# Kernel tuning notes

Measured on AMD Instinct MI355X. Metric: run time of the kernel, lower is better.

Reference implementation:

```python
import jax, jax.numpy as jnp
import numpy as np

N_NODES = 50000
N_EDGES = 800000
NFEAT = 96
NHID = 128
EPS = 1e-12  # F.normalize default eps


def setup_inputs() -> dict:
    key = jax.random.key(0)
    k1, k2, k3, k4 = jax.random.split(key, 4)
    edge_index = jax.random.randint(k1, (2, N_EDGES), 0, N_NODES, dtype=jnp.int64)
    x = jax.random.normal(k2, (N_NODES, NFEAT), dtype=jnp.float32)
    # Glorot-ish scaling for linear weights
    W_l = jax.random.normal(k3, (NHID, NFEAT), dtype=jnp.float32) * (1.0 / np.sqrt(NFEAT))
    b_l = jnp.zeros((NHID,), dtype=jnp.float32)
    W_r = jax.random.normal(k4, (NHID, NFEAT), dtype=jnp.float32) * (1.0 / np.sqrt(NFEAT))
    return {"edge_index": edge_index, "x": x, "W_l": W_l, "b_l": b_l, "W_r": W_r}


def reference(edge_index, x, W_l, b_l, W_r):
    # PyG SAGEConv, aggr='mean', root_weight=True, normalize=True
    src, dst = edge_index[0], edge_index[1]
    # gather source features, scatter-sum into destination nodes
    msg_sum = jax.ops.segment_sum(x[src], dst, num_segments=N_NODES)  # [N, nfeat]
    deg = jax.ops.segment_sum(jnp.ones((edge_index.shape[1],), dtype=x.dtype),
                              dst, num_segments=N_NODES)
    agg = msg_sum / jnp.maximum(deg, 1.0)[:, None]  # mean; isolated nodes -> 0
    out = agg @ W_l.T + b_l + x @ W_r.T  # [N, nhid]
    # L2 normalize per node (F.normalize p=2, dim=-1)
    norm = jnp.linalg.norm(out, axis=-1, keepdims=True)
    return out / jnp.maximum(norm, EPS)
```

## Files before the change

### kernel.cpp

```cpp
#include <hip/hip_runtime.h>


typedef __attribute__((ext_vector_type(8))) short short8;
typedef __attribute__((ext_vector_type(4))) float floatx4;

constexpr int kNodes = 50000;
constexpr int kEdges = 800000;
constexpr int kF = 96;
constexpr int kH = 128;
constexpr int kEllW = 32;
constexpr int kSpillCap = 4096;
constexpr int kBktRange = kNodes / 8;

constexpr size_t kXhOff    = 0;
constexpr size_t kAggOff   = 9600000;
constexpr size_t kWhOff    = 19200000;
constexpr size_t kEllOff   = 19249152;
constexpr size_t kCurOff   = 22449152;
constexpr size_t kSpcOff   = 22649152;
constexpr size_t kSpillOff = 22649168;

constexpr int kPeriods    = 782;
constexpr int kMegaBlocks = kPeriods * 11;
constexpr int kPrepBlocks = kPeriods * 3;
constexpr int kPrepItems  = kNodes * kF / 8 + kH * 192 / 8;
constexpr int kPrepStride = kPrepBlocks * 256;

__device__ __forceinline__ unsigned pack2_bf16(float a, float b) {
  unsigned ua = __float_as_uint(a), ub = __float_as_uint(b);
  ua = (ua + 0x7fffu + ((ua >> 16) & 1u)) >> 16;
  ub = (ub + 0x7fffu + ((ub >> 16) & 1u)) >> 16;
  return ua | (ub << 16);
}
__device__ __forceinline__ float bf_lo(unsigned u) { return __uint_as_float(u << 16); }
__device__ __forceinline__ float bf_hi(unsigned u) { return __uint_as_float(u & 0xffff0000u); }

__device__ __forceinline__ void ell_insert(int dst, int src, int* cursor,
                                           ushort* ell, unsigned* spill,
                                           int* spillCnt) {
  const int slot = atomicAdd(&cursor[dst], 1);
  if (slot < kEllW) {
    ell[(size_t)dst * kEllW + slot] = (ushort)src;
  } else {
    const int sp = atomicAdd(spillCnt, 1);
    if (sp < kSpillCap) spill[sp] = ((unsigned)dst << 16) | (unsigned)src;
  }
}

__global__ void __launch_bounds__(256)
mega_kernel(const int* __restrict__ ei, const float* __restrict__ x,
            const float* __restrict__ Wl, const float* __restrict__ Wr,
            uint4* __restrict__ xh4, uint4* __restrict__ wh4,
            int* __restrict__ cursor, ushort* __restrict__ ell,
            unsigned* __restrict__ spill, int* __restrict__ spillCnt) {
  const int p = blockIdx.x / 11;
  const int r = blockIdx.x % 11;
  if (r < 8) {
    const int g = r;
    const int lo = g * kBktRange, hi = lo + kBktRange;
    const int base = p * 1024 + threadIdx.x;
    int d[4];
#pragma unroll
    for (int k = 0; k < 4; ++k) {
      const int e = base + k * 256;
      d[k] = (e < kEdges) ? ei[kEdges + e] : -1;
    }
#pragma unroll
    for (int k = 0; k < 4; ++k) {
      if (d[k] >= lo && d[k] < hi) {
        const int e = base + k * 256;
        ell_insert(d[k], ei[e], cursor, ell, spill, spillCnt);
      }
    }
    return;
  }
  constexpr int kCvt = kNodes * kF / 8;
  const int pid = p * 3 + (r - 8);
  for (int i = pid * 256 + threadIdx.x; i < kPrepItems; i += kPrepStride) {
    if (i < kCvt) {
      const float4 v0 = reinterpret_cast<const float4*>(x)[i * 2];
      const float4 v1 = reinterpret_cast<const float4*>(x)[i * 2 + 1];
      uint4 o;
      o.x = pack2_bf16(v0.x, v0.y);
      o.y = pack2_bf16(v0.z, v0.w);
      o.z = pack2_bf16(v1.x, v1.y);
      o.w = pack2_bf16(v1.z, v1.w);
      xh4[i] = o;
    } else {
      const int j = i - kCvt;
      const int row = j / 24, chunk = j % 24;
      const float* src = (chunk < 12) ? (Wl + (size_t)row * kF + chunk * 8)
                                      : (Wr + (size_t)row * kF + (chunk - 12) * 8);
      const float4 v0 = reinterpret_cast<const float4*>(src)[0];
      const float4 v1 = reinterpret_cast<const float4*>(src)[1];
      uint4 o;
      o.x = pack2_bf16(v0.x, v0.y);
      o.y = pack2_bf16(v0.z, v0.w);
      o.z = pack2_bf16(v1.x, v1.y);
      o.w = pack2_bf16(v1.z, v1.w);
      wh4[j] = o;
    }
  }
}

__global__ void __launch_bounds__(256)
gather_kernel(const uint4* __restrict__ xh4, const int* __restrict__ cursor,
              const ushort* __restrict__ ell, const unsigned* __restrict__ spill,
              const int* __restrict__ spillCnt, uint4* __restrict__ aggh4) {
  const int wave = threadIdx.x >> 6, lane = threadIdx.x & 63;
  const int slot = lane / 12;
  const int c = lane % 12;
  const bool gactive = lane < 48;
  const int sc = min(*spillCnt, kSpillCap);
  const int g = blockIdx.x & 7;
  const int j = blockIdx.x >> 3;
  const int stride = (gridDim.x >> 3) * 8;
  const int hi = (g + 1) * kBktRange;

  for (int nA = g * kBktRange + j * 8 + wave * 2; nA < hi; nA += stride) {
    const int nB = nA + 1;
    const bool hasB = nB < hi;
    const int degA = cursor[nA];
    const int degB = hasB ? cursor[nB] : 0;
    const int dmA = min(degA, kEllW);
    const int dmB = min(degB, kEllW);
    const ushort* __restrict__ erowA = ell + (size_t)nA * kEllW;
    const ushort* __restrict__ erowB = ell + (size_t)nB * kEllW;

    float a0 = 0.f, a1 = 0.f, a2 = 0.f, a3 = 0.f,
          a4 = 0.f, a5 = 0.f, a6 = 0.f, a7 = 0.f;
    float b0 = 0.f, b1 = 0.f, b2 = 0.f, b3 = 0.f,
          b4 = 0.f, b5 = 0.f, b6 = 0.f, b7 = 0.f;

    int sA[8], sB[8];
#pragma unroll
    for (int t = 0; t < 8; ++t) {
      const int idx = (t << 2) + slot;
      sA[t] = (gactive && idx < dmA) ? (int)erowA[idx] : -1;
      sB[t] = (gactive && idx < dmB) ? (int)erowB[idx] : -1;
    }
#pragma unroll
    for (int t = 0; t < 8; ++t) {
      if (sA[t] >= 0) {
        const uint4 v = xh4[(size_t)sA[t] * 12 + c];
        a0 += bf_lo(v.x); a1 += bf_hi(v.x);
        a2 += bf_lo(v.y); a3 += bf_hi(v.y);
        a4 += bf_lo(v.z); a5 += bf_hi(v.z);
        a6 += bf_lo(v.w); a7 += bf_hi(v.w);
      }
      if (sB[t] >= 0) {
        const uint4 v = xh4[(size_t)sB[t] * 12 + c];
        b0 += bf_lo(v.x); b1 += bf_hi(v.x);
        b2 += bf_lo(v.y); b3 += bf_hi(v.y);
        b4 += bf_lo(v.z); b5 += bf_hi(v.z);
        b6 += bf_lo(v.w); b7 += bf_hi(v.w);
      }
    }
    for (int jj = 0; jj < sc; ++jj) {
      const unsigned pr = spill[jj];
      const int pd = (int)(pr >> 16);
      if (lane < 12 && (pd == nA || (hasB && pd == nB))) {
        const uint4 v = xh4[(size_t)(pr & 0xffffu) * 12 + c];
        if (pd == nA) {
          a0 += bf_lo(v.x); a1 += bf_hi(v.x);
          a2 += bf_lo(v.y); a3 += bf_hi(v.y);
          a4 += bf_lo(v.z); a5 += bf_hi(v.z);
          a6 += bf_lo(v.w); a7 += bf_hi(v.w);
        } else {
          b0 += bf_lo(v.x); b1 += bf_hi(v.x);
          b2 += bf_lo(v.y); b3 += bf_hi(v.y);
          b4 += bf_lo(v.z); b5 += bf_hi(v.z);
          b6 += bf_lo(v.w); b7 += bf_hi(v.w);
        }
      }
    }
    a0 += __shfl(a0, lane + 24, 64); a1 += __shfl(a1, lane + 24, 64);
    a2 += __shfl(a2, lane + 24, 64); a3 += __shfl(a3, lane + 24, 64);
    a4 += __shfl(a4, lane + 24, 64); a5 += __shfl(a5, lane + 24, 64);
    a6 += __shfl(a6, lane + 24, 64); a7 += __shfl(a7, lane + 24, 64);
    a0 += __shfl(a0, lane + 12, 64); a1 += __shfl(a1, lane + 12, 64);
    a2 += __shfl(a2, lane + 12, 64); a3 += __shfl(a3, lane + 12, 64);
    a4 += __shfl(a4, lane + 12, 64); a5 += __shfl(a5, lane + 12, 64);
    a6 += __shfl(a6, lane + 12, 64); a7 += __shfl(a7, lane + 12, 64);
    b0 += __shfl(b0, lane + 24, 64); b1 += __shfl(b1, lane + 24, 64);
    b2 += __shfl(b2, lane + 24, 64); b3 += __shfl(b3, lane + 24, 64);
    b4 += __shfl(b4, lane + 24, 64); b5 += __shfl(b5, lane + 24, 64);
    b6 += __shfl(b6, lane + 24, 64); b7 += __shfl(b7, lane + 24, 64);
    b0 += __shfl(b0, lane + 12, 64); b1 += __shfl(b1, lane + 12, 64);
    b2 += __shfl(b2, lane + 12, 64); b3 += __shfl(b3, lane + 12, 64);
    b4 += __shfl(b4, lane + 12, 64); b5 += __shfl(b5, lane + 12, 64);
    b6 += __shfl(b6, lane + 12, 64); b7 += __shfl(b7, lane + 12, 64);

    if (lane < 12) {
      const float invA = 1.0f / fmaxf((float)degA, 1.0f);
      uint4 o;
      o.x = pack2_bf16(a0 * invA, a1 * invA);
      o.y = pack2_bf16(a2 * invA, a3 * invA);
      o.z = pack2_bf16(a4 * invA, a5 * invA);
      o.w = pack2_bf16(a6 * invA, a7 * invA);
      aggh4[(size_t)nA * 12 + c] = o;
      if (hasB) {
        const float invB = 1.0f / fmaxf((float)degB, 1.0f);
        uint4 p;
        p.x = pack2_bf16(b0 * invB, b1 * invB);
        p.y = pack2_bf16(b2 * invB, b3 * invB);
        p.z = pack2_bf16(b4 * invB, b5 * invB);
        p.w = pack2_bf16(b6 * invB, b7 * invB);
        aggh4[(size_t)nB * 12 + c] = p;
      }
    }
  }
}

__global__ void __launch_bounds__(256)
mfma_kernel(const uint4* __restrict__ xh4, const uint4* __restrict__ aggh4,
            const uint4* __restrict__ wh4, const float* __restrict__ bl,
            float* __restrict__ out) {
  const int wave = threadIdx.x >> 6, lane = threadIdx.x & 63;
  const int tile = blockIdx.x * 4 + wave;
  if (tile >= kNodes / 16) return;
  const int base = tile * 16;
  const int r = lane & 15, q = lane >> 4;

  const short8* aggS = reinterpret_cast<const short8*>(aggh4);
  const short8* xhS  = reinterpret_cast<const short8*>(xh4);
  const short8* whS  = reinterpret_cast<const short8*>(wh4);

  floatx4 acc[8] = {};
#pragma unroll
  for (int ks = 0; ks < 6; ++ks) {
    const short8* Ab = (ks < 3) ? aggS : xhS;
    const int chunk = (ks < 3 ? ks * 4 : (ks - 3) * 4) + q;
    const short8 a = Ab[(size_t)(base + r) * 12 + chunk];
#pragma unroll
    for (int cg = 0; cg < 8; ++cg) {
      const short8 b = whS[(cg * 16 + r) * 24 + ks * 4 + q];
      acc[cg] = __builtin_amdgcn_mfma_f32_16x16x32_bf16(a, b, acc[cg], 0, 0, 0);
    }
  }

  float p0 = 0.f, p1 = 0.f, p2 = 0.f, p3 = 0.f;
#pragma unroll
  for (int cg = 0; cg < 8; ++cg) {
    const float bb = bl[cg * 16 + r];
    acc[cg][0] += bb; acc[cg][1] += bb; acc[cg][2] += bb; acc[cg][3] += bb;
    p0 += acc[cg][0] * acc[cg][0];
    p1 += acc[cg][1] * acc[cg][1];
    p2 += acc[cg][2] * acc[cg][2];
    p3 += acc[cg][3] * acc[cg][3];
  }
#pragma unroll
  for (int off = 1; off < 16; off <<= 1) {
    p0 += __shfl_xor(p0, off, 64);
    p1 += __shfl_xor(p1, off, 64);
    p2 += __shfl_xor(p2, off, 64);
    p3 += __shfl_xor(p3, off, 64);
  }
  const float s0 = 1.0f / fmaxf(sqrtf(p0), 1e-12f);
  const float s1 = 1.0f / fmaxf(sqrtf(p1), 1e-12f);
  const float s2 = 1.0f / fmaxf(sqrtf(p2), 1e-12f);
  const float s3 = 1.0f / fmaxf(sqrtf(p3), 1e-12f);

#pragma unroll
  for (int cg = 0; cg < 8; ++cg) {
    const int col = cg * 16 + r;
    float* o = out + (size_t)(base + q * 4) * kH + col;
    o[0 * kH] = acc[cg][0] * s0;
    o[1 * kH] = acc[cg][1] * s1;
    o[2 * kH] = acc[cg][2] * s2;
    o[3 * kH] = acc[cg][3] * s3;
  }
}

extern "C" void kernel_launch(void* const* d_in, const int* in_sizes, int n_in,
                              void* d_out, int out_size, void* d_ws, size_t ws_size,
                              hipStream_t stream) {
  const int*   ei = (const int*)d_in[0];
  const float* x  = (const float*)d_in[1];
  const float* Wl = (const float*)d_in[2];
  const float* bl = (const float*)d_in[3];
  const float* Wr = (const float*)d_in[4];
  float* out = (float*)d_out;

  char* ws = (char*)d_ws;
  uint4*    xh4      = (uint4*)(ws + kXhOff);
  uint4*    aggh4    = (uint4*)(ws + kAggOff);
  uint4*    wh4      = (uint4*)(ws + kWhOff);
  ushort*   ell      = (ushort*)(ws + kEllOff);
  int*      cursor   = (int*)(ws + kCurOff);
  int*      spillCnt = (int*)(ws + kSpcOff);
  unsigned* spill    = (unsigned*)(ws + kSpillOff);

  hipMemsetAsync(ws + kCurOff, 0, 200008, stream);

  mega_kernel<<<kMegaBlocks, 256, 0, stream>>>(ei, x, Wl, Wr, xh4, wh4, cursor,
                                               ell, spill, spillCnt);

  gather_kernel<<<391 * 8, 256, 0, stream>>>(xh4, cursor, ell, spill, spillCnt,
                                             aggh4);

  constexpr int tiles = kNodes / 16;
  mfma_kernel<<<(tiles + 3) / 4, 256, 0, stream>>>(xh4, aggh4, wh4, bl, out);
}
```

Measured before the change: 112.6 us.

## Fuse neighbor gather into MFMA kernel via per-wave LDS aggregate tile

Merges the gather and MFMA kernels: each wave aggregates neighbor means for its 16-node tile into a padded shared-memory buffer, then feeds those rows straight into the bf16 MFMA projection. This removes one kernel launch and the round trip of the aggregated bf16 tensor through global memory. In exchange, the gather loses its node-bucketed scheduling, which may have aimed at cache locality, the grid shrinks to one block per 64 nodes, and LDS use per block could reduce occupancy.

```diff
diff --git a/kernel.cpp b/kernel.cpp
--- a/kernel.cpp
+++ b/kernel.cpp
@@ -13,7 +13,6 @@
 constexpr int kBktRange = kNodes / 8;
 
 constexpr size_t kXhOff    = 0;
-constexpr size_t kAggOff   = 9600000;
 constexpr size_t kWhOff    = 19200000;
 constexpr size_t kEllOff   = 19249152;
 constexpr size_t kCurOff   = 22449152;
@@ -25,6 +24,8 @@
 constexpr int kPrepBlocks = kPeriods * 3;
 constexpr int kPrepItems  = kNodes * kF / 8 + kH * 192 / 8;
 constexpr int kPrepStride = kPrepBlocks * 256;
+
+constexpr int kRowS = 104;
 
 __device__ __forceinline__ unsigned pack2_bf16(float a, float b) {
   unsigned ua = __float_as_uint(a), ub = __float_as_uint(b);
@@ -104,24 +105,28 @@
 }
 
 __global__ void __launch_bounds__(256)
-gather_kernel(const uint4* __restrict__ xh4, const int* __restrict__ cursor,
-              const ushort* __restrict__ ell, const unsigned* __restrict__ spill,
-              const int* __restrict__ spillCnt, uint4* __restrict__ aggh4) {
+gm_kernel(const uint4* __restrict__ xh4, const int* __restrict__ cursor,
+          const ushort* __restrict__ ell, const unsigned* __restrict__ spill,
+          const int* __restrict__ spillCnt, const uint4* __restrict__ wh4,
+          const float* __restrict__ bl, float* __restrict__ out) {
+  __shared__ __align__(16) short sAgg[4][16 * kRowS];
+
   const int wave = threadIdx.x >> 6, lane = threadIdx.x & 63;
+  const int tile = blockIdx.x * 4 + wave;
+  if (tile >= kNodes / 16) return;
+  const int base = tile * 16;
+
   const int slot = lane / 12;
   const int c = lane % 12;
   const bool gactive = lane < 48;
   const int sc = min(*spillCnt, kSpillCap);
-  const int g = blockIdx.x & 7;
-  const int j = blockIdx.x >> 3;
-  const int stride = (gridDim.x >> 3) * 8;
-  const int hi = (g + 1) * kBktRange;
-
-  for (int nA = g * kBktRange + j * 8 + wave * 2; nA < hi; nA += stride) {
+
+#pragma unroll
+  for (int it = 0; it < 8; ++it) {
+    const int nA = base + it * 2;
     const int nB = nA + 1;
-    const bool hasB = nB < hi;
     const int degA = cursor[nA];
-    const int degB = hasB ? cursor[nB] : 0;
+    const int degB = cursor[nB];
     const int dmA = min(degA, kEllW);
     const int dmB = min(degB, kEllW);
     const ushort* __restrict__ erowA = ell + (size_t)nA * kEllW;
@@ -159,7 +164,7 @@
     for (int jj = 0; jj < sc; ++jj) {
       const unsigned pr = spill[jj];
       const int pd = (int)(pr >> 16);
-      if (lane < 12 && (pd == nA || (hasB && pd == nB))) {
+      if (lane < 12 && (pd == nA || pd == nB)) {
         const uint4 v = xh4[(size_t)(pr & 0xffffu) * 12 + c];
         if (pd == nA) {
           a0 += bf_lo(v.x); a1 += bf_hi(v.x);
@@ -198,40 +203,31 @@
       o.y = pack2_bf16(a2 * invA, a3 * invA);
       o.z = pack2_bf16(a4 * invA, a5 * invA);
       o.w = pack2_bf16(a6 * invA, a7 * invA);
-      aggh4[(size_t)nA * 12 + c] = o;
-      if (hasB) {
-        const float invB = 1.0f / fmaxf((float)degB, 1.0f);
-        uint4 p;
-        p.x = pack2_bf16(b0 * invB, b1 * invB);
-        p.y = pack2_bf16(b2 * invB, b3 * invB);
-        p.z = pack2_bf16(b4 * invB, b5 * invB);
-        p.w = pack2_bf16(b6 * invB, b7 * invB);
-        aggh4[(size_t)nB * 12 + c] = p;
-      }
-    }
-  }
-}
-
-__global__ void __launch_bounds__(256)
-mfma_kernel(const uint4* __restrict__ xh4, const uint4* __restrict__ aggh4,
-            const uint4* __restrict__ wh4, const float* __restrict__ bl,
-            float* __restrict__ out) {
-  const int wave = threadIdx.x >> 6, lane = threadIdx.x & 63;
-  const int tile = blockIdx.x * 4 + wave;
-  if (tile >= kNodes / 16) return;
-  const int base = tile * 16;
+      *reinterpret_cast<uint4*>(&sAgg[wave][(it * 2) * kRowS + c * 8]) = o;
+      const float invB = 1.0f / fmaxf((float)degB, 1.0f);
+      uint4 p;
+      p.x = pack2_bf16(b0 * invB, b1 * invB);
+      p.y = pack2_bf16(b2 * invB, b3 * invB);
+      p.z = pack2_bf16(b4 * invB, b5 * invB);
+      p.w = pack2_bf16(b6 * invB, b7 * invB);
+      *reinterpret_cast<uint4*>(&sAgg[wave][(it * 2 + 1) * kRowS + c * 8]) = p;
+    }
+  }
+
   const int r = lane & 15, q = lane >> 4;
-
-  const short8* aggS = reinterpret_cast<const short8*>(aggh4);
-  const short8* xhS  = reinterpret_cast<const short8*>(xh4);
-  const short8* whS  = reinterpret_cast<const short8*>(wh4);
+  const short8* xhS = reinterpret_cast<const short8*>(xh4);
+  const short8* whS = reinterpret_cast<const short8*>(wh4);
 
   floatx4 acc[8] = {};
 #pragma unroll
   for (int ks = 0; ks < 6; ++ks) {
-    const short8* Ab = (ks < 3) ? aggS : xhS;
-    const int chunk = (ks < 3 ? ks * 4 : (ks - 3) * 4) + q;
-    const short8 a = Ab[(size_t)(base + r) * 12 + chunk];
+    short8 a;
+    if (ks < 3) {
+      a = *reinterpret_cast<const short8*>(
+          &sAgg[wave][r * kRowS + (ks * 4 + q) * 8]);
+    } else {
+      a = xhS[(size_t)(base + r) * 12 + (ks - 3) * 4 + q];
+    }
 #pragma unroll
     for (int cg = 0; cg < 8; ++cg) {
       const short8 b = whS[(cg * 16 + r) * 24 + ks * 4 + q];
@@ -284,7 +280,6 @@
 
   char* ws = (char*)d_ws;
   uint4*    xh4      = (uint4*)(ws + kXhOff);
-  uint4*    aggh4    = (uint4*)(ws + kAggOff);
   uint4*    wh4      = (uint4*)(ws + kWhOff);
   ushort*   ell      = (ushort*)(ws + kEllOff);
   int*      cursor   = (int*)(ws + kCurOff);
@@ -296,9 +291,7 @@
   mega_kernel<<<kMegaBlocks, 256, 0, stream>>>(ei, x, Wl, Wr, xh4, wh4, cursor,
                                                ell, spill, spillCnt);
 
-  gather_kernel<<<391 * 8, 256, 0, stream>>>(xh4, cursor, ell, spill, spillCnt,
-                                             aggh4);
-
   constexpr int tiles = kNodes / 16;
-  mfma_kernel<<<(tiles + 3) / 4, 256, 0, stream>>>(xh4, aggh4, wh4, bl, out);
-}
+  gm_kernel<<<(tiles + 3) / 4, 256, 0, stream>>>(xh4, cursor, ell, spill,
+                                                 spillCnt, wh4, bl, out);
+}
```

After: 123.6 us. 1.1x slower.
